# Kernel tuning notes

Measured on AMD Instinct MI355X. Metric: run time of the kernel, lower is better.

## Reference

```python
import jax, jax.numpy as jnp
import numpy as np

NUM_CLASSES = 13
HIDDEN = 64
NUM_LAYERS = 2
NODE_FEAT = 1 + 4 + NUM_CLASSES  # 18
N_NODES = 100000
N_EDGES = 1600000


def _glorot(key, shape):
    fan_in, fan_out = shape[0], shape[1]
    lim = (6.0 / (fan_in + fan_out)) ** 0.5
    return jax.random.uniform(key, shape, jnp.float32, -lim, lim)


def setup_inputs() -> dict:
    key = jax.random.key(0)
    ks = jax.random.split(key, 32)
    H = HIDDEN
    inp = {
        "node_features": jax.random.normal(ks[0], (N_NODES, NODE_FEAT), jnp.float32),
        "edge_index": jax.random.randint(ks[1], (2, N_EDGES), 0, N_NODES, jnp.int32),
        "edge_weights": jax.random.uniform(ks[2], (N_EDGES,), jnp.float32),
        "embed_W": _glorot(ks[3], (NODE_FEAT, H)),
        "embed_b": jnp.zeros((H,), jnp.float32),
        # stacked per-layer params, leading dim = NUM_LAYERS
        "msg_W1": jnp.stack([_glorot(ks[4 + i], (2 * H, H)) for i in range(NUM_LAYERS)]),
        "msg_b1": jnp.zeros((NUM_LAYERS, H), jnp.float32),
        "msg_W2": jnp.stack([_glorot(ks[8 + i], (H, H)) for i in range(NUM_LAYERS)]),
        "msg_b2": jnp.zeros((NUM_LAYERS, H), jnp.float32),
        "att_W1": jnp.stack([_glorot(ks[12 + i], (2 * H, H // 2)) for i in range(NUM_LAYERS)]),
        "att_b1": jnp.zeros((NUM_LAYERS, H // 2), jnp.float32),
        "att_W2": jnp.stack([_glorot(ks[16 + i], (H // 2, 1)) for i in range(NUM_LAYERS)]),
        "att_b2": jnp.zeros((NUM_LAYERS, 1), jnp.float32),
        "upd_W1": jnp.stack([_glorot(ks[20 + i], (2 * H, H)) for i in range(NUM_LAYERS)]),
        "upd_b1": jnp.zeros((NUM_LAYERS, H), jnp.float32),
        "upd_W2": jnp.stack([_glorot(ks[24 + i], (H, H)) for i in range(NUM_LAYERS)]),
        "upd_b2": jnp.zeros((NUM_LAYERS, H), jnp.float32),
        "head_W": _glorot(ks[28], (H, 1)),
        "head_b": jnp.zeros((1,), jnp.float32),
    }
    return inp


def _mlp2(x, W1, b1, W2, b2):
    return jax.nn.relu(x @ W1 + b1) @ W2 + b2


def reference(node_features, edge_index, edge_weights,
              embed_W, embed_b,
              msg_W1, msg_b1, msg_W2, msg_b2,
              att_W1, att_b1, att_W2, att_b2,
              upd_W1, upd_b1, upd_W2, upd_b2,
              head_W, head_b):
    row, col = edge_index[0], edge_index[1]
    x = jax.nn.relu(node_features @ embed_W + embed_b)  # [N, H]
    num_nodes = x.shape[0]
    for l in range(NUM_LAYERS):
        cat = jnp.concatenate([x[row], x[col]], axis=-1)  # [E, 2H]
        messages = _mlp2(cat, msg_W1[l], msg_b1[l], msg_W2[l], msg_b2[l])  # [E, H]
        att = jax.nn.sigmoid(_mlp2(cat, att_W1[l], att_b1[l], att_W2[l], att_b2[l])[:, 0])  # [E]
        fw = edge_weights * att
        messages = messages * fw[:, None]
        aggregated = jax.ops.segment_sum(messages, col, num_segments=num_nodes)  # [N, H]
        norm = jax.ops.segment_sum(fw, col, num_segments=num_nodes)
        norm = jnp.clip(norm, 1e-6, None)
        aggregated = aggregated / norm[:, None]
        x_new = _mlp2(jnp.concatenate([x, aggregated], axis=-1),
                      upd_W1[l], upd_b1[l], upd_W2[l], upd_b2[l])
        x = jax.nn.relu(x_new + x)
    series_repr = jnp.max(x, axis=0)  # [H]
    binary_logit = (series_repr @ head_W + head_b)[0]
    return binary_logit
```

## Files before the change

kernel.cpp:

```cpp
#include <hip/hip_runtime.h>
#include <hip/hip_bf16.h>
#include <math.h>

#define H 64
#define F 18
#define NPW 2
#define NBKT 1024
#define EPB 8192

typedef _Float16 f16x8 __attribute__((ext_vector_type(8)));
typedef _Float16 f16x4 __attribute__((ext_vector_type(4)));
typedef _Float16 f16x2 __attribute__((ext_vector_type(2)));
typedef __fp16 h16x2 __attribute__((ext_vector_type(2)));
typedef float f32x4 __attribute__((ext_vector_type(4)));

__global__ __launch_bounds__(256) void embed_kernel(
    const float* __restrict__ nf, const float* __restrict__ W,
    const float* __restrict__ b, _Float16* __restrict__ xh, int N)
{
    int n = blockIdx.x * 256 + threadIdx.x;
    if (n >= N) return;
    float acc[H];
#pragma unroll
    for (int j = 0; j < H; ++j) acc[j] = b[j];
    const float* f = nf + (long)n * F;
#pragma unroll
    for (int i = 0; i < F; ++i) {
        float c = f[i];
        const float* w = W + i * H;
#pragma unroll
        for (int j = 0; j < H; ++j) acc[j] += c * w[j];
    }
    union { uint4 v[8]; _Float16 h[64]; } O;
#pragma unroll
    for (int j = 0; j < H; ++j) O.h[j] = (_Float16)fmaxf(acc[j], 0.f);
    uint4* xo = (uint4*)(xh + (size_t)n * H);
#pragma unroll
    for (int i = 0; i < 8; ++i) xo[i] = O.v[i];
}

__global__ __launch_bounds__(256) void packfrag_uv_kernel(
    const float* __restrict__ mW1, const float* __restrict__ aW1,
    f16x8* __restrict__ uvB)
{
    int t = blockIdx.x * 256 + threadIdx.x;
    if (t >= 3072) return;
    int lane = t & 63;
    int frag = t >> 6;
    int l = frag / 24, rem = frag % 24;
    int side = rem / 12, q = rem % 12;
    int nt = q >> 1, kk = q & 1;
    int quad = lane >> 4, l15 = lane & 15;
    int col = nt * 16 + l15;
    f16x8 v;
#pragma unroll
    for (int j = 0; j < 8; ++j) {
        int k = side * 64 + kk * 32 + quad * 8 + j;
        float w = (col < 64) ? mW1[(size_t)l * 8192 + k * 64 + col]
                             : aW1[(size_t)l * 4096 + k * 32 + (col - 64)];
        v[j] = (_Float16)w;
    }
    uvB[(size_t)frag * 64 + lane] = v;
}

__global__ __launch_bounds__(256) void prep_update_kernel(
    const float* __restrict__ mW2, const float* __restrict__ mb2,
    const float* __restrict__ uW1,
    float* __restrict__ M2U, float* __restrict__ mbu)
{
    int t = blockIdx.x * 256 + threadIdx.x;
    if (t >= 2 * 64 * 64) return;
    int l = t >> 12, r = t & 4095;
    int i = r >> 6, j = r & 63;
    const float* W2 = mW2 + (size_t)l * 4096;
    const float* U1b = uW1 + (size_t)l * 8192 + 4096;
    float s = 0.f;
    for (int k = 0; k < 64; ++k) s += W2[i * 64 + k] * U1b[k * 64 + j];
    M2U[t] = s;
    if (i == 0) {
        float sb = 0.f;
        const float* b2 = mb2 + (size_t)l * 64;
        for (int k = 0; k < 64; ++k) sb += b2[k] * U1b[k * 64 + j];
        mbu[l * 64 + j] = sb;
    }
}

__global__ __launch_bounds__(256) void packfrag_upd_kernel(
    const float* __restrict__ uW1, const float* __restrict__ M2U,
    const float* __restrict__ uW2, f16x8* __restrict__ updB)
{
    int t = blockIdx.x * 256 + threadIdx.x;
    if (t >= 3072) return;
    int lane = t & 63;
    int frag = t >> 6;
    int l = frag / 24, f = frag % 24;
    int quad = lane >> 4, l15 = lane & 15;
    int g = f >> 3, ff = f & 7;
    int nt = ff >> 1, kk = ff & 1;
    const float* src;
    if (g == 0)      src = uW1 + (size_t)l * 8192;
    else if (g == 1) src = M2U + (size_t)l * 4096;
    else             src = uW2 + (size_t)l * 4096;
    f16x8 v;
#pragma unroll
    for (int j = 0; j < 8; ++j) {
        int k = kk * 32 + quad * 8 + j;
        v[j] = (_Float16)src[k * 64 + nt * 16 + l15];
    }
    updB[(size_t)frag * 64 + lane] = v;
}

__global__ __launch_bounds__(256) void scan1_kernel(
    const int* __restrict__ deg, int* __restrict__ part,
    int* __restrict__ bsum, int N)
{
    __shared__ int lds[256];
    int t = threadIdx.x;
    int base = blockIdx.x * 1024 + t * 4;
    int v[4];
#pragma unroll
    for (int s = 0; s < 4; ++s) v[s] = (base + s < N) ? deg[base + s] : 0;
    int sum = v[0] + v[1] + v[2] + v[3];
    lds[t] = sum;
    __syncthreads();
    for (int off = 1; off < 256; off <<= 1) {
        int xv = (t >= off) ? lds[t - off] : 0;
        __syncthreads();
        lds[t] += xv;
        __syncthreads();
    }
    int excl = lds[t] - sum;
    if (t == 255) bsum[blockIdx.x] = lds[255];
    int p = excl;
#pragma unroll
    for (int s = 0; s < 4; ++s) {
        if (base + s < N) part[base + s] = p;
        p += v[s];
    }
}

__global__ __launch_bounds__(256) void scan2_kernel(int* __restrict__ bsum, int nb)
{
    __shared__ int lds[256];
    int t = threadIdx.x;
    int v = (t < nb) ? bsum[t] : 0;
    lds[t] = v;
    __syncthreads();
    for (int off = 1; off < 256; off <<= 1) {
        int xv = (t >= off) ? lds[t - off] : 0;
        __syncthreads();
        lds[t] += xv;
        __syncthreads();
    }
    if (t < nb) bsum[t] = lds[t] - v;
}

__global__ __launch_bounds__(256) void scan3_kernel(
    int* __restrict__ part, const int* __restrict__ bsum, int N)
{
    int i = blockIdx.x * 256 + threadIdx.x;
    if (i >= N) return;
    part[i] = part[i] + bsum[i >> 10];
}

__global__ __launch_bounds__(256) void count_bucket_kernel(
    const int* __restrict__ col, int* __restrict__ cnt,
    unsigned int* __restrict__ serp, int E, int NB, int NBK, int BS)
{
    __shared__ int lc[NBKT];
    int t = threadIdx.x;
    if (blockIdx.x == 0 && t < 64) serp[t] = 0;
    for (int i = t; i < NBK; i += 256) lc[i] = 0;
    __syncthreads();
    for (int s = 0; s < EPB / 256; ++s) {
        int e = blockIdx.x * EPB + s * 256 + t;
        if (e < E) atomicAdd(lc + (unsigned)col[e] / (unsigned)BS, 1);
    }
    __syncthreads();
    for (int i = t; i < NBK; i += 256)
        cnt[(size_t)i * NB + blockIdx.x] = lc[i];
}

__global__ __launch_bounds__(256) void place_kernel(
    const int* __restrict__ row, const int* __restrict__ col,
    const float* __restrict__ ew, const int* __restrict__ off,
    int2* __restrict__ edata, int E, int NB, int NBK, int BS)
{
    __shared__ int lc[NBKT];
    int t = threadIdx.x;
    for (int i = t; i < NBK; i += 256) lc[i] = 0;
    __syncthreads();
    for (int s = 0; s < EPB / 256; ++s) {
        int e = blockIdx.x * EPB + s * 256 + t;
        if (e < E) {
            int cv = col[e];
            int c = (unsigned)cv / (unsigned)BS;
            int lcol = cv - c * BS;
            int r = atomicAdd(lc + c, 1);
            int pos = off[(size_t)c * NB + blockIdx.x] + r;
            edata[pos] = make_int2(row[e] | (lcol << 20), __float_as_int(ew[e]));
        }
    }
}

__global__ __launch_bounds__(256) void bucket_sort_kernel(
    int2* __restrict__ edata, const int* __restrict__ off,
    int* __restrict__ deg, int* __restrict__ startp,
    int NB, int BS, int N, int E, int NBK)
{
    __shared__ int hist[256];
    __shared__ int psum[256];
    int b = blockIdx.x;
    int t = threadIdx.x;
    int base = off[(size_t)b * NB];
    int end  = (b + 1 < NBK) ? off[(size_t)(b + 1) * NB] : E;
    int cnt = end - base;
    int nlo = b * BS;

    hist[t] = 0;
    __syncthreads();

    int2 regs[8];
    int lnode[8];
#pragma unroll
    for (int ii = 0; ii < 8; ++ii) {
        int i = t + ii * 256;
        if (i < cnt) {
            regs[ii] = edata[base + i];
            lnode[ii] = ((unsigned)regs[ii].x) >> 20;
            atomicAdd(hist + lnode[ii], 1);
        }
    }
    __syncthreads();

    int cv = hist[t];
    psum[t] = cv;
    __syncthreads();
    for (int o = 1; o < 256; o <<= 1) {
        int xv = (t >= o) ? psum[t - o] : 0;
        __syncthreads();
        psum[t] += xv;
        __syncthreads();
    }
    int excl = psum[t] - cv;
    int ng = nlo + t;
    if (t < BS && ng < N) {
        deg[ng] = cv;
        startp[ng] = base + excl;
    }
    hist[t] = excl;
    __syncthreads();

#pragma unroll
    for (int ii = 0; ii < 8; ++ii) {
        int i = t + ii * 256;
        if (i < cnt) {
            int pos = atomicAdd(hist + lnode[ii], 1);
            edata[base + pos] = make_int2(regs[ii].x & 0xFFFFF, regs[ii].y);
        }
    }
}

__global__ __launch_bounds__(256) void uv_mfma_kernel(
    const _Float16* __restrict__ xh, const f16x8* __restrict__ Bf,
    const float* __restrict__ mb1, const float* __restrict__ ab1,
    _Float16* __restrict__ UV, int N, int nbside)
{
    int bid = blockIdx.x;
    int side = (bid >= nbside) ? 1 : 0;
    int b = bid - side * nbside;
    int lane = threadIdx.x & 63;
    int wid = (b * 256 + (int)threadIdx.x) >> 6;
    int quad = lane >> 4, l15 = lane & 15;
    int nbase = wid * 64;
    if (nbase >= N) return;

    const f16x8* Bs = Bf + side * 12 * 64;
    f16x8 B[12];
#pragma unroll
    for (int i = 0; i < 12; ++i) B[i] = Bs[i * 64 + lane];
    float bv[6];
#pragma unroll
    for (int nt = 0; nt < 6; ++nt) {
        int col = nt * 16 + l15;
        bv[nt] = side ? 0.f : (col < 64 ? mb1[col] : ab1[col - 64]);
    }

    for (int mt = 0; mt < 4; ++mt) {
        int na = nbase + mt * 16 + l15;
        if (na >= N) na = N - 1;
        const f16x8* xrow = (const f16x8*)(xh + (size_t)na * H);
        f16x8 Ax[2];
        Ax[0] = xrow[quad];
        Ax[1] = xrow[4 + quad];

        f32x4 C[6];
#pragma unroll
        for (int nt = 0; nt < 6; ++nt) {
            f32x4 cc = {bv[nt], bv[nt], bv[nt], bv[nt]};
#pragma unroll
            for (int kk = 0; kk < 2; ++kk)
                cc = __builtin_amdgcn_mfma_f32_16x16x32_f16(Ax[kk], B[nt * 2 + kk], cc, 0, 0, 0);
            C[nt] = cc;
        }
#pragma unroll
        for (int r = 0; r < 4; ++r) {
            int n = nbase + mt * 16 + quad * 4 + r;
            if (n < N) {
#pragma unroll
                for (int nt = 0; nt < 6; ++nt)
                    UV[(size_t)n * 192 + side * 96 + nt * 16 + l15] = (_Float16)C[nt][r];
            }
        }
    }
}

__global__ __launch_bounds__(256) void edge_gather_kernel(
    const _Float16* __restrict__ UV,
    const int2* __restrict__ edata,
    const int* __restrict__ startp, const int* __restrict__ deg,
    const float* __restrict__ aW2, const float* __restrict__ ab2,
    _Float16* __restrict__ aggN, float* __restrict__ snorm, int N)
{
    int wid = (blockIdx.x * 256 + threadIdx.x) >> 6;
    int lane = threadIdx.x & 63;
    int g = lane >> 3, s = lane & 7;
    int n0 = wid * NPW;
    if (n0 >= N) return;
    int n1 = n0 + NPW; if (n1 > N) n1 = N;

    float aw2v[4];
#pragma unroll
    for (int j = 0; j < 4; ++j) aw2v[j] = aW2[s * 4 + j];
#if __has_builtin(__builtin_amdgcn_fdot2)
    h16x2 aw01, aw23;
    aw01[0] = (__fp16)aw2v[0]; aw01[1] = (__fp16)aw2v[1];
    aw23[0] = (__fp16)aw2v[2]; aw23[1] = (__fp16)aw2v[3];
#endif
    float ab2v = ab2[0];
    const f16x2 zer = {(_Float16)0, (_Float16)0};

    typedef union { f16x8 v; f16x2 p[4]; } u8p;
    typedef union { f16x4 v; f16x2 p[2]; h16x2 h[2]; } u4p;

    for (int n = n0; n < n1; ++n) {
        int e0 = startp[n];
        int d = deg[n];
        int iters = (d + 7) >> 3;
        const _Float16* vrow = UV + (size_t)n * 192 + 96;
        u8p vm; vm.v = *(const f16x8*)(vrow + s * 8);
        u4p va; va.v = *(const f16x4*)(vrow + 64 + s * 4);

        float acc[8];
#pragma unroll
        for (int j = 0; j < 8; ++j) acc[j] = 0.f;
        float rfw = 0.f;

        if (iters > 0) {
            int2 ed0, ed1 = {0, 0}, ed2 = {0, 0};
            u8p um0;
            u4p ua0;
            {
                int ei = g;
                ed0 = edata[e0 + (ei < d ? ei : 0)];
                const _Float16* ur = UV + (size_t)ed0.x * 192;
                um0.v = *(const f16x8*)(ur + s * 8);
                ua0.v = *(const f16x4*)(ur + 64 + s * 4);
            }
            if (iters > 1) {
                int ei = 8 + g;
                ed1 = edata[e0 + (ei < d ? ei : 0)];
            }
            for (int it = 0; it < iters; ++it) {
                u8p umn = um0;
                u4p uan = ua0;
                if (it + 1 < iters) {
                    const _Float16* ur = UV + (size_t)ed1.x * 192;
                    umn.v = *(const f16x8*)(ur + s * 8);
                    uan.v = *(const f16x4*)(ur + 64 + s * 4);
                }
                if (it + 2 < iters) {
                    int ei = (it + 2) * 8 + g;
                    ed2 = edata[e0 + (ei < d ? ei : 0)];
                }

                int ei = it * 8 + g;
                float ew = (ei < d) ? __int_as_float(ed0.y) : 0.f;
                f16x2 za0 = __builtin_elementwise_max(ua0.p[0] + va.p[0], zer);
                f16x2 za1 = __builtin_elementwise_max(ua0.p[1] + va.p[1], zer);
#if __has_builtin(__builtin_amdgcn_fdot2)
                h16x2 hz0, hz1;
                __builtin_memcpy(&hz0, &za0, 4);
                __builtin_memcpy(&hz1, &za1, 4);
                float pp = __builtin_amdgcn_fdot2(
                    hz0, aw01,
                    __builtin_amdgcn_fdot2(hz1, aw23, 0.f, false), false);
#else
                float pp = (float)za0[0] * aw2v[0] + (float)za0[1] * aw2v[1]
                         + (float)za1[0] * aw2v[2] + (float)za1[1] * aw2v[3];
#endif
                pp += __int_as_float(__builtin_amdgcn_update_dpp(
                    0, __float_as_int(pp), 0xB1, 0xF, 0xF, true));
                pp += __int_as_float(__builtin_amdgcn_update_dpp(
                    0, __float_as_int(pp), 0x4E, 0xF, 0xF, true));
                pp += __shfl_xor(pp, 4);
                float fw = ew * __builtin_amdgcn_rcpf(1.f + __expf(-(pp + ab2v)));
#pragma unroll
                for (int j = 0; j < 4; ++j) {
                    f16x2 z = __builtin_elementwise_max(um0.p[j] + vm.p[j], zer);
                    acc[2 * j]     += (float)z[0] * fw;
                    acc[2 * j + 1] += (float)z[1] * fw;
                }
                rfw += fw;

                ed0 = ed1; ed1 = ed2; um0 = umn; ua0 = uan;
            }
        }

#pragma unroll
        for (int o = 8; o <= 32; o <<= 1) {
#pragma unroll
            for (int j = 0; j < 8; ++j) acc[j] += __shfl_xor(acc[j], o);
            rfw += __shfl_xor(rfw, o);
        }
        float inv = 1.f / fmaxf(rfw, 1e-6f);
        if (g == 0) {
            union { _Float16 h[8]; uint4 v; } O;
#pragma unroll
            for (int j = 0; j < 8; ++j) O.h[j] = (_Float16)(acc[j] * inv);
            *(uint4*)(aggN + (size_t)n * H + s * 8) = O.v;
        }
        if (lane == 0) snorm[n] = rfw * inv;
    }
}

__global__ __launch_bounds__(64, 2) void update_mfma_kernel(
    _Float16* __restrict__ xh, const _Float16* __restrict__ agg,
    const float* __restrict__ snorm,
    const f16x8* __restrict__ Bfrag,
    const float* __restrict__ mbu,
    const float* __restrict__ ub1, const float* __restrict__ ub2,
    const f16x8* __restrict__ uvBn,
    const float* __restrict__ mb1n, const float* __restrict__ ab1n,
    _Float16* __restrict__ UV,
    unsigned int* __restrict__ serp,
    int N, int doMax)
{
    __shared__ __align__(16) _Float16 hlds[16 * 80];
    int lane = threadIdx.x;
    int wid = blockIdx.x;
    int quad = lane >> 4, l15 = lane & 15;
    int nbase = wid * 64;
    if (nbase >= N) return;

    f16x8 Bu[8], Bm[8], Bw[8];
#pragma unroll
    for (int i = 0; i < 8; ++i) {
        Bu[i] = Bfrag[i * 64 + lane];
        Bm[i] = Bfrag[(8 + i) * 64 + lane];
        Bw[i] = Bfrag[(16 + i) * 64 + lane];
    }
    float mbuv[4], b1v[4], b2v[4];
#pragma unroll
    for (int nt = 0; nt < 4; ++nt) {
        mbuv[nt] = mbu[nt * 16 + l15];
        b1v[nt] = ub1[nt * 16 + l15];
        b2v[nt] = ub2[nt * 16 + l15];
    }
    float bvn[12];
    if (uvBn) {
#pragma unroll
        for (int q = 0; q < 12; ++q) {
            int sd = q / 6, nt2 = q % 6;
            int col = nt2 * 16 + l15;
            bvn[q] = sd ? 0.f : (col < 64 ? mb1n[col] : ab1n[col - 64]);
        }
    }
    float lmax[4] = {0.f, 0.f, 0.f, 0.f};

    for (int mt = 0; mt < 4; ++mt) {
        int na = nbase + mt * 16 + l15;
        if (na >= N) na = N - 1;
        const f16x8* xrow = (const f16x8*)(xh + (size_t)na * H);
        f16x8 Ax[2];
        Ax[0] = xrow[quad];
        Ax[1] = xrow[4 + quad];
        const f16x8* arow = (const f16x8*)(agg + (size_t)na * H);
        f16x8 Aa[2];
        Aa[0] = arow[quad];
        Aa[1] = arow[4 + quad];

        f32x4 Cx[4], Ca[4];
#pragma unroll
        for (int nt = 0; nt < 4; ++nt) {
            f32x4 cx = {0.f, 0.f, 0.f, 0.f}, ca = {0.f, 0.f, 0.f, 0.f};
#pragma unroll
            for (int kk = 0; kk < 2; ++kk) {
                cx = __builtin_amdgcn_mfma_f32_16x16x32_f16(Ax[kk], Bu[nt * 2 + kk], cx, 0, 0, 0);
                ca = __builtin_amdgcn_mfma_f32_16x16x32_f16(Aa[kk], Bm[nt * 2 + kk], ca, 0, 0, 0);
            }
            Cx[nt] = cx; Ca[nt] = ca;
        }

        int noder = nbase + mt * 16 + quad * 4;
        float sn_r[4];
#pragma unroll
        for (int r = 0; r < 4; ++r) {
            int ng = noder + r; if (ng >= N) ng = N - 1;
            sn_r[r] = snorm[ng];
        }

#pragma unroll
        for (int nt = 0; nt < 4; ++nt) {
#pragma unroll
            for (int r = 0; r < 4; ++r) {
                float hv = fmaxf(Cx[nt][r] + Ca[nt][r]
                                 + sn_r[r] * mbuv[nt] + b1v[nt], 0.f);
                hlds[(quad * 4 + r) * 80 + nt * 16 + l15] = (_Float16)hv;
            }
        }
        __asm__ __volatile__("s_waitcnt lgkmcnt(0)" ::: "memory");
        f16x8 Ah[2];
        Ah[0] = *(const f16x8*)&hlds[l15 * 80 + quad * 8];
        Ah[1] = *(const f16x8*)&hlds[l15 * 80 + 32 + quad * 8];
        __asm__ __volatile__("s_waitcnt lgkmcnt(0)" ::: "memory");

        f32x4 C2[4];
#pragma unroll
        for (int nt = 0; nt < 4; ++nt) {
            f32x4 cc = {0.f, 0.f, 0.f, 0.f};
#pragma unroll
            for (int kk = 0; kk < 2; ++kk)
                cc = __builtin_amdgcn_mfma_f32_16x16x32_f16(Ah[kk], Bw[nt * 2 + kk], cc, 0, 0, 0);
            C2[nt] = cc;
        }

        float xn[4][4];
#pragma unroll
        for (int r = 0; r < 4; ++r) {
            int ng = noder + r;
            if (ng < N) {
#pragma unroll
                for (int nt = 0; nt < 4; ++nt) {
                    size_t idx = (size_t)ng * H + nt * 16 + l15;
                    float xo = (float)xh[idx];
                    float v = fmaxf(C2[nt][r] + b2v[nt] + xo, 0.f);
                    xn[nt][r] = v;
                    xh[idx] = (_Float16)v;
                }
            } else {
#pragma unroll
                for (int nt = 0; nt < 4; ++nt) xn[nt][r] = 0.f;
            }
        }
        if (doMax) {
#pragma unroll
            for (int nt = 0; nt < 4; ++nt)
#pragma unroll
                for (int r = 0; r < 4; ++r) lmax[nt] = fmaxf(lmax[nt], xn[nt][r]);
        }

        if (uvBn) {
#pragma unroll
            for (int nt = 0; nt < 4; ++nt)
#pragma unroll
                for (int r = 0; r < 4; ++r)
                    hlds[(quad * 4 + r) * 80 + nt * 16 + l15] = (_Float16)xn[nt][r];
            __asm__ __volatile__("s_waitcnt lgkmcnt(0)" ::: "memory");
            f16x8 A2[2];
            A2[0] = *(const f16x8*)&hlds[l15 * 80 + quad * 8];
            A2[1] = *(const f16x8*)&hlds[l15 * 80 + 32 + quad * 8];
            __asm__ __volatile__("s_waitcnt lgkmcnt(0)" ::: "memory");

#pragma unroll
            for (int q = 0; q < 12; ++q) {
                int sd = q / 6, nt2 = q % 6;
                f16x8 Ba = uvBn[(sd * 12 + nt2 * 2) * 64 + lane];
                f16x8 Bb = uvBn[(sd * 12 + nt2 * 2 + 1) * 64 + lane];
                f32x4 cc = {bvn[q], bvn[q], bvn[q], bvn[q]};
                cc = __builtin_amdgcn_mfma_f32_16x16x32_f16(A2[0], Ba, cc, 0, 0, 0);
                cc = __builtin_amdgcn_mfma_f32_16x16x32_f16(A2[1], Bb, cc, 0, 0, 0);
#pragma unroll
                for (int r = 0; r < 4; ++r) {
                    int n = noder + r;
                    if (n < N)
                        UV[(size_t)n * 192 + sd * 96 + nt2 * 16 + l15] = (_Float16)cc[r];
                }
            }
        }
    }

    if (doMax) {
#pragma unroll
        for (int nt = 0; nt < 4; ++nt) {
            float m = lmax[nt];
            m = fmaxf(m, __shfl_xor(m, 16));
            m = fmaxf(m, __shfl_xor(m, 32));
            if (quad == 0) atomicMax(serp + nt * 16 + l15, __float_as_uint(m));
        }
    }
}

__global__ void head_kernel(const unsigned int* __restrict__ serp,
                            const float* __restrict__ hW,
                            const float* __restrict__ hb,
                            float* __restrict__ out)
{
    int j = threadIdx.x;
    float v = __uint_as_float(serp[j]) * hW[j];
#pragma unroll
    for (int off = 32; off > 0; off >>= 1) v += __shfl_down(v, off);
    if (j == 0) out[0] = v + hb[0];
}

extern "C" void kernel_launch(void* const* d_in, const int* in_sizes, int n_in,
                              void* d_out, int out_size, void* d_ws, size_t ws_size,
                              hipStream_t stream)
{
    const float* nf  = (const float*)d_in[0];
    const int*   ei  = (const int*)d_in[1];
    const float* ew  = (const float*)d_in[2];
    const float* eW  = (const float*)d_in[3];
    const float* eb_ = (const float*)d_in[4];
    const float* mW1 = (const float*)d_in[5];
    const float* mb1 = (const float*)d_in[6];
    const float* mW2 = (const float*)d_in[7];
    const float* mb2 = (const float*)d_in[8];
    const float* aW1 = (const float*)d_in[9];
    const float* ab1 = (const float*)d_in[10];
    const float* aW2 = (const float*)d_in[11];
    const float* ab2 = (const float*)d_in[12];
    const float* uW1 = (const float*)d_in[13];
    const float* ub1 = (const float*)d_in[14];
    const float* uW2 = (const float*)d_in[15];
    const float* ub2 = (const float*)d_in[16];
    const float* hW  = (const float*)d_in[17];
    const float* hb  = (const float*)d_in[18];

    int N = in_sizes[0] / F;
    int E = in_sizes[2];
    const int* row = ei;
    const int* col = ei + E;

    size_t Nr = ((size_t)N + 3) & ~(size_t)3;
    size_t Er = ((size_t)E + 3) & ~(size_t)3;

    int BS  = (N + NBKT - 1) / NBKT;
    int NBK = (N + BS - 1) / BS;
    int NB  = (E + EPB - 1) / EPB;
    size_t M  = (size_t)NBK * NB;
    size_t Mr = (M + 3) & ~(size_t)3;

    _Float16* xh   = (_Float16*)d_ws;
    _Float16* aggN = xh + Nr * 64;
    float* snorm   = (float*)(aggN + Nr * 64);
    unsigned int* serp = (unsigned int*)(snorm + Nr);
    int* deg       = (int*)(serp + 64);
    int* startp    = deg + Nr;
    int* bsum      = startp + Nr;
    float* M2U     = (float*)(bsum + 256);
    float* mbu     = M2U + 8192;
    f16x8* updB    = (f16x8*)(mbu + 128);
    f16x8* uvB     = updB + 3072;
    _Float16* UV   = (_Float16*)(uvB + 3072);
    int* cnt       = (int*)(UV + Nr * 192);
    int* off       = cnt + Mr;
    int2* edata    = (int2*)(off + Mr);

    int nb_n = (N + 255) / 256;
    int nbA = (int)((M + 1023) / 1024);

    count_bucket_kernel<<<NB, 256, 0, stream>>>(col, cnt, serp, E, NB, NBK, BS);
    scan1_kernel<<<nbA, 256, 0, stream>>>(cnt, off, bsum, (int)M);
    scan2_kernel<<<1, 256, 0, stream>>>(bsum, nbA);
    scan3_kernel<<<(int)((M + 255) / 256), 256, 0, stream>>>(off, bsum, (int)M);
    place_kernel<<<NB, 256, 0, stream>>>(row, col, ew, off, edata, E, NB, NBK, BS);
    bucket_sort_kernel<<<NBK, 256, 0, stream>>>(edata, off, deg, startp,
                                                NB, BS, N, E, NBK);

    packfrag_uv_kernel<<<12, 256, 0, stream>>>(mW1, aW1, uvB);
    prep_update_kernel<<<32, 256, 0, stream>>>(mW2, mb2, uW1, M2U, mbu);
    packfrag_upd_kernel<<<12, 256, 0, stream>>>(uW1, M2U, uW2, updB);
    embed_kernel<<<nb_n, 256, 0, stream>>>(nf, eW, eb_, xh, N);

    int nwaves_n = (N + 63) / 64;
    int nb_uv = (N + 255) / 256;
    int nb_eg = (N + NPW * 4 - 1) / (NPW * 4);

    uv_mfma_kernel<<<2 * nb_uv, 256, 0, stream>>>(
        xh, uvB, mb1, ab1, UV, N, nb_uv);
    edge_gather_kernel<<<nb_eg, 256, 0, stream>>>(
        UV, edata, startp, deg, aW2, ab2, aggN, snorm, N);
    update_mfma_kernel<<<nwaves_n, 64, 0, stream>>>(
        xh, aggN, snorm, updB, mbu, ub1, ub2,
        uvB + 24 * 64, mb1 + H, ab1 + (H / 2), UV, nullptr, N, 0);
    edge_gather_kernel<<<nb_eg, 256, 0, stream>>>(
        UV, edata, startp, deg, aW2 + (H / 2), ab2 + 1, aggN, snorm, N);
    update_mfma_kernel<<<nwaves_n, 64, 0, stream>>>(
        xh, aggN, snorm, updB + 24 * 64, mbu + 64, ub1 + H, ub2 + H,
        nullptr, nullptr, nullptr, nullptr, serp, N, 1);

    head_kernel<<<1, 64, 0, stream>>>(serp, hW, hb, (float*)d_out);
}
```

Baseline: 389.8 us.

## Fuse embedding into UV MFMA kernel and fold scan3 into consumers

Replaces the scalar embed kernel and the separate UV MFMA kernel with one kernel. It computes the embedding with MFMA, writes xh, stages the activations through LDS and immediately computes both UV sides, so xh is not re-read from global memory. It also removes the scan3 pass by having place and bucket_sort add the block prefix sum on the fly, and merges the two weight-packing kernels into one. The cost is more registers per wave (launch bounds 64,2 with 24 B fragments held) and a per-wave LDS round trip. Both UV sides are now computed by a single wave per 64 nodes instead of being split across blocks.

```diff
diff --git a/kernel.cpp b/kernel.cpp
--- a/kernel.cpp
+++ b/kernel.cpp
@@ -13,55 +13,6 @@
 typedef _Float16 f16x2 __attribute__((ext_vector_type(2)));
 typedef __fp16 h16x2 __attribute__((ext_vector_type(2)));
 typedef float f32x4 __attribute__((ext_vector_type(4)));
-
-__global__ __launch_bounds__(256) void embed_kernel(
-    const float* __restrict__ nf, const float* __restrict__ W,
-    const float* __restrict__ b, _Float16* __restrict__ xh, int N)
-{
-    int n = blockIdx.x * 256 + threadIdx.x;
-    if (n >= N) return;
-    float acc[H];
-#pragma unroll
-    for (int j = 0; j < H; ++j) acc[j] = b[j];
-    const float* f = nf + (long)n * F;
-#pragma unroll
-    for (int i = 0; i < F; ++i) {
-        float c = f[i];
-        const float* w = W + i * H;
-#pragma unroll
-        for (int j = 0; j < H; ++j) acc[j] += c * w[j];
-    }
-    union { uint4 v[8]; _Float16 h[64]; } O;
-#pragma unroll
-    for (int j = 0; j < H; ++j) O.h[j] = (_Float16)fmaxf(acc[j], 0.f);
-    uint4* xo = (uint4*)(xh + (size_t)n * H);
-#pragma unroll
-    for (int i = 0; i < 8; ++i) xo[i] = O.v[i];
-}
-
-__global__ __launch_bounds__(256) void packfrag_uv_kernel(
-    const float* __restrict__ mW1, const float* __restrict__ aW1,
-    f16x8* __restrict__ uvB)
-{
-    int t = blockIdx.x * 256 + threadIdx.x;
-    if (t >= 3072) return;
-    int lane = t & 63;
-    int frag = t >> 6;
-    int l = frag / 24, rem = frag % 24;
-    int side = rem / 12, q = rem % 12;
-    int nt = q >> 1, kk = q & 1;
-    int quad = lane >> 4, l15 = lane & 15;
-    int col = nt * 16 + l15;
-    f16x8 v;
-#pragma unroll
-    for (int j = 0; j < 8; ++j) {
-        int k = side * 64 + kk * 32 + quad * 8 + j;
-        float w = (col < 64) ? mW1[(size_t)l * 8192 + k * 64 + col]
-                             : aW1[(size_t)l * 4096 + k * 32 + (col - 64)];
-        v[j] = (_Float16)w;
-    }
-    uvB[(size_t)frag * 64 + lane] = v;
-}
 
 __global__ __launch_bounds__(256) void prep_update_kernel(
     const float* __restrict__ mW2, const float* __restrict__ mb2,
@@ -85,29 +36,58 @@
     }
 }
 
-__global__ __launch_bounds__(256) void packfrag_upd_kernel(
+__global__ __launch_bounds__(256) void packfrag_all_kernel(
+    const float* __restrict__ mW1, const float* __restrict__ aW1,
     const float* __restrict__ uW1, const float* __restrict__ M2U,
-    const float* __restrict__ uW2, f16x8* __restrict__ updB)
+    const float* __restrict__ uW2, const float* __restrict__ eW,
+    f16x8* __restrict__ uvB, f16x8* __restrict__ updB,
+    f16x8* __restrict__ embB)
 {
     int t = blockIdx.x * 256 + threadIdx.x;
-    if (t >= 3072) return;
+    if (t >= 6400) return;
     int lane = t & 63;
     int frag = t >> 6;
-    int l = frag / 24, f = frag % 24;
     int quad = lane >> 4, l15 = lane & 15;
-    int g = f >> 3, ff = f & 7;
-    int nt = ff >> 1, kk = ff & 1;
-    const float* src;
-    if (g == 0)      src = uW1 + (size_t)l * 8192;
-    else if (g == 1) src = M2U + (size_t)l * 4096;
-    else             src = uW2 + (size_t)l * 4096;
-    f16x8 v;
-#pragma unroll
-    for (int j = 0; j < 8; ++j) {
-        int k = kk * 32 + quad * 8 + j;
-        v[j] = (_Float16)src[k * 64 + nt * 16 + l15];
-    }
-    updB[(size_t)frag * 64 + lane] = v;
+    if (frag < 48) {
+        int l = frag / 24, rem = frag % 24;
+        int side = rem / 12, q = rem % 12;
+        int nt = q >> 1, kk = q & 1;
+        int col = nt * 16 + l15;
+        f16x8 v;
+#pragma unroll
+        for (int j = 0; j < 8; ++j) {
+            int k = side * 64 + kk * 32 + quad * 8 + j;
+            float w = (col < 64) ? mW1[(size_t)l * 8192 + k * 64 + col]
+                                 : aW1[(size_t)l * 4096 + k * 32 + (col - 64)];
+            v[j] = (_Float16)w;
+        }
+        uvB[(size_t)frag * 64 + lane] = v;
+    } else if (frag < 96) {
+        int f2 = frag - 48;
+        int l = f2 / 24, f = f2 % 24;
+        int g = f >> 3, ff = f & 7;
+        int nt = ff >> 1, kk = ff & 1;
+        const float* src;
+        if (g == 0)      src = uW1 + (size_t)l * 8192;
+        else if (g == 1) src = M2U + (size_t)l * 4096;
+        else             src = uW2 + (size_t)l * 4096;
+        f16x8 v;
+#pragma unroll
+        for (int j = 0; j < 8; ++j) {
+            int k = kk * 32 + quad * 8 + j;
+            v[j] = (_Float16)src[k * 64 + nt * 16 + l15];
+        }
+        updB[(size_t)f2 * 64 + lane] = v;
+    } else {
+        int nt = frag - 96;
+        f16x8 v;
+#pragma unroll
+        for (int j = 0; j < 8; ++j) {
+            int k = quad * 8 + j;
+            v[j] = (k < F) ? (_Float16)eW[k * 64 + nt * 16 + l15] : (_Float16)0;
+        }
+        embB[(size_t)nt * 64 + lane] = v;
+    }
 }
 
 __global__ __launch_bounds__(256) void scan1_kernel(
@@ -155,14 +135,6 @@
     if (t < nb) bsum[t] = lds[t] - v;
 }
 
-__global__ __launch_bounds__(256) void scan3_kernel(
-    int* __restrict__ part, const int* __restrict__ bsum, int N)
-{
-    int i = blockIdx.x * 256 + threadIdx.x;
-    if (i >= N) return;
-    part[i] = part[i] + bsum[i >> 10];
-}
-
 __global__ __launch_bounds__(256) void count_bucket_kernel(
     const int* __restrict__ col, int* __restrict__ cnt,
     unsigned int* __restrict__ serp, int E, int NB, int NBK, int BS)
@@ -184,6 +156,7 @@
 __global__ __launch_bounds__(256) void place_kernel(
     const int* __restrict__ row, const int* __restrict__ col,
     const float* __restrict__ ew, const int* __restrict__ off,
+    const int* __restrict__ bsum,
     int2* __restrict__ edata, int E, int NB, int NBK, int BS)
 {
     __shared__ int lc[NBKT];
@@ -197,7 +170,8 @@
             int c = (unsigned)cv / (unsigned)BS;
             int lcol = cv - c * BS;
             int r = atomicAdd(lc + c, 1);
-            int pos = off[(size_t)c * NB + blockIdx.x] + r;
+            int idx = c * NB + blockIdx.x;
+            int pos = off[idx] + bsum[idx >> 10] + r;
             edata[pos] = make_int2(row[e] | (lcol << 20), __float_as_int(ew[e]));
         }
     }
@@ -205,6 +179,7 @@
 
 __global__ __launch_bounds__(256) void bucket_sort_kernel(
     int2* __restrict__ edata, const int* __restrict__ off,
+    const int* __restrict__ bsum,
     int* __restrict__ deg, int* __restrict__ startp,
     int NB, int BS, int N, int E, int NBK)
 {
@@ -212,8 +187,13 @@
     __shared__ int psum[256];
     int b = blockIdx.x;
     int t = threadIdx.x;
-    int base = off[(size_t)b * NB];
-    int end  = (b + 1 < NBK) ? off[(size_t)(b + 1) * NB] : E;
+    int i0 = b * NB;
+    int base = off[i0] + bsum[i0 >> 10];
+    int end = E;
+    if (b + 1 < NBK) {
+        int i1 = (b + 1) * NB;
+        end = off[i1] + bsum[i1 >> 10];
+    }
     int cnt = end - base;
     int nlo = b * BS;
 
@@ -261,55 +241,90 @@
     }
 }
 
-__global__ __launch_bounds__(256) void uv_mfma_kernel(
-    const _Float16* __restrict__ xh, const f16x8* __restrict__ Bf,
+__global__ __launch_bounds__(64, 2) void embed_uv_kernel(
+    const float* __restrict__ nf, const f16x8* __restrict__ embB,
+    const float* __restrict__ eb,
+    const f16x8* __restrict__ uvB0,
     const float* __restrict__ mb1, const float* __restrict__ ab1,
-    _Float16* __restrict__ UV, int N, int nbside)
-{
-    int bid = blockIdx.x;
-    int side = (bid >= nbside) ? 1 : 0;
-    int b = bid - side * nbside;
-    int lane = threadIdx.x & 63;
-    int wid = (b * 256 + (int)threadIdx.x) >> 6;
+    _Float16* __restrict__ xh, _Float16* __restrict__ UV, int N)
+{
+    __shared__ __align__(16) _Float16 hlds[16 * 80];
+    int lane = threadIdx.x;
+    int wid = blockIdx.x;
     int quad = lane >> 4, l15 = lane & 15;
     int nbase = wid * 64;
     if (nbase >= N) return;
 
-    const f16x8* Bs = Bf + side * 12 * 64;
-    f16x8 B[12];
-#pragma unroll
-    for (int i = 0; i < 12; ++i) B[i] = Bs[i * 64 + lane];
-    float bv[6];
-#pragma unroll
-    for (int nt = 0; nt < 6; ++nt) {
-        int col = nt * 16 + l15;
-        bv[nt] = side ? 0.f : (col < 64 ? mb1[col] : ab1[col - 64]);
+    f16x8 Be[4];
+#pragma unroll
+    for (int i = 0; i < 4; ++i) Be[i] = embB[i * 64 + lane];
+    f16x8 B[24];
+#pragma unroll
+    for (int i = 0; i < 24; ++i) B[i] = uvB0[i * 64 + lane];
+    float bve[4];
+#pragma unroll
+    for (int nt = 0; nt < 4; ++nt) bve[nt] = eb[nt * 16 + l15];
+    float bvn[12];
+#pragma unroll
+    for (int q = 0; q < 12; ++q) {
+        int sd = q / 6, nt2 = q % 6;
+        int col = nt2 * 16 + l15;
+        bvn[q] = sd ? 0.f : (col < 64 ? mb1[col] : ab1[col - 64]);
     }
 
     for (int mt = 0; mt < 4; ++mt) {
         int na = nbase + mt * 16 + l15;
         if (na >= N) na = N - 1;
-        const f16x8* xrow = (const f16x8*)(xh + (size_t)na * H);
-        f16x8 Ax[2];
-        Ax[0] = xrow[quad];
-        Ax[1] = xrow[4 + quad];
-
-        f32x4 C[6];
-#pragma unroll
-        for (int nt = 0; nt < 6; ++nt) {
-            f32x4 cc = {bv[nt], bv[nt], bv[nt], bv[nt]};
-#pragma unroll
-            for (int kk = 0; kk < 2; ++kk)
-                cc = __builtin_amdgcn_mfma_f32_16x16x32_f16(Ax[kk], B[nt * 2 + kk], cc, 0, 0, 0);
+        f16x8 Ax;
+#pragma unroll
+        for (int j = 0; j < 8; ++j) {
+            int k = quad * 8 + j;
+            Ax[j] = (k < F) ? (_Float16)nf[(size_t)na * F + k] : (_Float16)0;
+        }
+
+        f32x4 C[4];
+#pragma unroll
+        for (int nt = 0; nt < 4; ++nt) {
+            f32x4 cc = {bve[nt], bve[nt], bve[nt], bve[nt]};
+            cc = __builtin_amdgcn_mfma_f32_16x16x32_f16(Ax, Be[nt], cc, 0, 0, 0);
             C[nt] = cc;
         }
+
+        int noder = nbase + mt * 16 + quad * 4;
+        float xn[4][4];
 #pragma unroll
         for (int r = 0; r < 4; ++r) {
-            int n = nbase + mt * 16 + quad * 4 + r;
-            if (n < N) {
-#pragma unroll
-                for (int nt = 0; nt < 6; ++nt)
-                    UV[(size_t)n * 192 + side * 96 + nt * 16 + l15] = (_Float16)C[nt][r];
+            int ng = noder + r;
+#pragma unroll
+            for (int nt = 0; nt < 4; ++nt) {
+                float v = fmaxf(C[nt][r], 0.f);
+                xn[nt][r] = v;
+                if (ng < N) xh[(size_t)ng * H + nt * 16 + l15] = (_Float16)v;
+            }
+        }
+
+#pragma unroll
+        for (int nt = 0; nt < 4; ++nt)
+#pragma unroll
+            for (int r = 0; r < 4; ++r)
+                hlds[(quad * 4 + r) * 80 + nt * 16 + l15] = (_Float16)xn[nt][r];
+        __asm__ __volatile__("s_waitcnt lgkmcnt(0)" ::: "memory");
+        f16x8 A2[2];
+        A2[0] = *(const f16x8*)&hlds[l15 * 80 + quad * 8];
+        A2[1] = *(const f16x8*)&hlds[l15 * 80 + 32 + quad * 8];
+        __asm__ __volatile__("s_waitcnt lgkmcnt(0)" ::: "memory");
+
+#pragma unroll
+        for (int q = 0; q < 12; ++q) {
+            int sd = q / 6, nt2 = q % 6;
+            f32x4 cc = {bvn[q], bvn[q], bvn[q], bvn[q]};
+            cc = __builtin_amdgcn_mfma_f32_16x16x32_f16(A2[0], B[sd * 12 + nt2 * 2], cc, 0, 0, 0);
+            cc = __builtin_amdgcn_mfma_f32_16x16x32_f16(A2[1], B[sd * 12 + nt2 * 2 + 1], cc, 0, 0, 0);
+#pragma unroll
+            for (int r = 0; r < 4; ++r) {
+                int n = noder + r;
+                if (n < N)
+                    UV[(size_t)n * 192 + sd * 96 + nt2 * 16 + l15] = (_Float16)cc[r];
             }
         }
     }
@@ -662,33 +677,30 @@
     float* mbu     = M2U + 8192;
     f16x8* updB    = (f16x8*)(mbu + 128);
     f16x8* uvB     = updB + 3072;
-    _Float16* UV   = (_Float16*)(uvB + 3072);
+    f16x8* embB    = uvB + 3072;
+    _Float16* UV   = (_Float16*)(embB + 256);
     int* cnt       = (int*)(UV + Nr * 192);
     int* off       = cnt + Mr;
     int2* edata    = (int2*)(off + Mr);
 
-    int nb_n = (N + 255) / 256;
     int nbA = (int)((M + 1023) / 1024);
 
     count_bucket_kernel<<<NB, 256, 0, stream>>>(col, cnt, serp, E, NB, NBK, BS);
     scan1_kernel<<<nbA, 256, 0, stream>>>(cnt, off, bsum, (int)M);
     scan2_kernel<<<1, 256, 0, stream>>>(bsum, nbA);
-    scan3_kernel<<<(int)((M + 255) / 256), 256, 0, stream>>>(off, bsum, (int)M);
-    place_kernel<<<NB, 256, 0, stream>>>(row, col, ew, off, edata, E, NB, NBK, BS);
-    bucket_sort_kernel<<<NBK, 256, 0, stream>>>(edata, off, deg, startp,
+    place_kernel<<<NB, 256, 0, stream>>>(row, col, ew, off, bsum, edata, E, NB, NBK, BS);
+    bucket_sort_kernel<<<NBK, 256, 0, stream>>>(edata, off, bsum, deg, startp,
                                                 NB, BS, N, E, NBK);
 
-    packfrag_uv_kernel<<<12, 256, 0, stream>>>(mW1, aW1, uvB);
     prep_update_kernel<<<32, 256, 0, stream>>>(mW2, mb2, uW1, M2U, mbu);
-    packfrag_upd_kernel<<<12, 256, 0, stream>>>(uW1, M2U, uW2, updB);
-    embed_kernel<<<nb_n, 256, 0, stream>>>(nf, eW, eb_, xh, N);
+    packfrag_all_kernel<<<25, 256, 0, stream>>>(mW1, aW1, uW1, M2U, uW2, eW,
+                                                uvB, updB, embB);
 
     int nwaves_n = (N + 63) / 64;
-    int nb_uv = (N + 255) / 256;
     int nb_eg = (N + NPW * 4 - 1) / (NPW * 4);
 
-    uv_mfma_kernel<<<2 * nb_uv, 256, 0, stream>>>(
-        xh, uvB, mb1, ab1, UV, N, nb_uv);
+    embed_uv_kernel<<<nwaves_n, 64, 0, stream>>>(
+        nf, embB, eb_, uvB, mb1, ab1, xh, UV, N);
     edge_gather_kernel<<<nb_eg, 256, 0, stream>>>(
         UV, edata, startp, deg, aW2, ab2, aggN, snorm, N);
     update_mfma_kernel<<<nwaves_n, 64, 0, stream>>>(
```

Measured after the change: 368.5 us. -5.5%, faster.
